# Kernel optimization log

Measured on AMD Instinct MI355X. Metric: run time of the kernel, lower is better.

The kernel has to match this reference:

```python
import jax, jax.numpy as jnp
import numpy as np

DIM = 1024
HEADS = 16
HD = DIM // HEADS          # 64
HID = 4 * DIM              # 4096
TPF = 1374                 # tokens_per_frame
LR = 0.1
NS_ITERS = 5
TTT_STEPS = 2
B, S = 2, 4
SN = S * TPF               # 5496


def _newton_schulz(G, iters=NS_ITERS):
    """Muon Newton-Schulz orthogonalization (quintic iteration)."""
    a, b, c = 3.4445, -4.7750, 2.0315
    X = G / (jnp.linalg.norm(G) + 1e-7)
    transposed = G.shape[0] > G.shape[1]
    if transposed:
        X = X.T
    for _ in range(iters):
        A = X @ X.T                      # [m,m], m = min(rows, cols)
        X = a * X + (b * A + c * (A @ A)) @ X
    return X.T if transposed else X


def _muon_update(p, g):
    return p - LR * _newton_schulz(g)


def setup_inputs() -> dict:
    key = jax.random.key(0)
    ks = jax.random.split(key, 8)
    inp = {
        "x": jax.random.normal(ks[0], (B, SN, DIM), jnp.float32),
        "qkv_w": jax.random.normal(ks[1], (DIM, 3 * DIM), jnp.float32) * (DIM ** -0.5),
        "qkv_b": jnp.zeros((3 * DIM,), jnp.float32),
        "qn_scale": jnp.ones((HD,), jnp.float32),
        "qn_bias": jnp.zeros((HD,), jnp.float32),
        "kn_scale": jnp.ones((HD,), jnp.float32),
        "kn_bias": jnp.zeros((HD,), jnp.float32),
        # theta: lecun-normal scale (std = 1/sqrt(fan_in))
        "ttt_gate": jax.random.normal(ks[2], (DIM, HID), jnp.float32) * (DIM ** -0.5),
        "ttt_val": jax.random.normal(ks[3], (DIM, HID), jnp.float32) * (DIM ** -0.5),
        "ttt_proj": jax.random.normal(ks[4], (HID, DIM), jnp.float32) * (HID ** -0.5),
        "proj_w": jax.random.normal(ks[5], (DIM, DIM), jnp.float32) * (DIM ** -0.5),
        "proj_b": jnp.zeros((DIM,), jnp.float32),
    }
    return inp


def reference(x, qkv_w, qkv_b, qn_scale, qn_bias, kn_scale, kn_bias,
              ttt_gate, ttt_val, ttt_proj, proj_w, proj_b):
    Bx, SNx, _ = x.shape
    qkv = x @ qkv_w + qkv_b                       # [B, SN, 3*DIM]
    q, k, v = jnp.split(qkv, 3, axis=-1)
    q = q.reshape(Bx, SNx, HEADS, HD)
    k = k.reshape(Bx, SNx, HEADS, HD)
    # per-head L2 normalize then affine NormLayer (x*scale + bias)
    q = q / (jnp.linalg.norm(q, axis=-1, keepdims=True) + 1e-6) * qn_scale + qn_bias
    k = k / (jnp.linalg.norm(k, axis=-1, keepdims=True) + 1e-6) * kn_scale + kn_bias
    q_ttt = q.reshape(-1, DIM)                    # [B*SN, DIM]
    k_ttt = k.reshape(-1, DIM)
    # no short_conv param at init -> v_mixed is identity, so v_target == v
    v_ttt = v.reshape(-1, DIM)

    theta = {"gate": ttt_gate, "val": ttt_val, "proj": ttt_proj}

    def loss_fn(p):
        h = jax.nn.swish(k_ttt @ p["gate"]) * (k_ttt @ p["val"])   # [B*SN, HID]
        pred = h @ p["proj"]                                        # [B*SN, DIM]
        return jnp.mean((pred - v_ttt) ** 2)

    for _ in range(TTT_STEPS):
        grads = jax.grad(loss_fn)(theta)
        theta = {kk: _muon_update(theta[kk], grads[kk]) for kk in theta}

    h_q = jax.nn.swish(q_ttt @ theta["gate"]) * (q_ttt @ theta["val"])
    o = (h_q @ theta["proj"]) @ proj_w + proj_b
    return o.reshape(Bx, SNx, DIM)
```

## Files before the change

### kernel.cpp

```cpp
#include <hip/hip_runtime.h>
#include <stdint.h>

#define NTOK 10992
#define NTOKA 11264
#define FCHK 5632
#define PMi 4194304

typedef unsigned short u16;
typedef __attribute__((ext_vector_type(8))) __bf16 b8;
typedef __attribute__((ext_vector_type(4))) float f32x4;

__device__ __forceinline__ u16 f2b(float f) {
  union { float f; uint32_t u; } v; v.f = f;
  return (u16)((v.u + 0x7fffu + ((v.u >> 16) & 1u)) >> 16);
}
__device__ __forceinline__ float b2f(u16 b) {
  union { uint32_t u; float f; } v; v.u = ((uint32_t)b) << 16; return v.f;
}
__device__ __forceinline__ uint2 pk4(u16 a, u16 b, u16 c, u16 d) {
  uint2 r; r.x = (uint32_t)a | ((uint32_t)b << 16); r.y = (uint32_t)c | ((uint32_t)d << 16);
  return r;
}
__device__ __forceinline__ void gload16(const u16* g, u16* l) {
  __builtin_amdgcn_global_load_lds((const __attribute__((address_space(1))) void*)(const void*)g,
                                   (__attribute__((address_space(3))) void*)(void*)l, 16, 0, 0);
}

struct GA {
  const u16* A[3]; const u16* B[3];
  void* C[3]; u16* O1[3]; u16* OT[3];
  const void* E0[3]; const u16* E1[3];
  int lda[3], ldb[3];
  int M, N, K, ldc, ldo1, ldt, lde0, lde1;
  float p0, p1;
};

template <int EPI, int SPLIT>
__global__ __launch_bounds__(256, 2) void gemm_bt(GA g) {
  __shared__ u16 As[128 * 32];
  __shared__ u16 Bs[128 * 32];
  int bz = blockIdx.z, koff = 0, klen = g.K;
  if constexpr (SPLIT) { koff = (bz & 1) * (g.K >> 1); bz >>= 1; klen = g.K >> 1; }
  const u16* __restrict__ A = g.A[bz] + koff;
  const u16* __restrict__ B = g.B[bz] + koff;
  const int lda = g.lda[bz], ldb = g.ldb[bz];
  const int m0 = blockIdx.y * 128, n0 = blockIdx.x * 128;
  const int tid = threadIdx.x, w = tid >> 6, lane = tid & 63;
  const int wr = (w >> 1) * 64, wc = (w & 1) * 64;
  const int ln = lane & 15, lq = lane >> 4;

  f32x4 acc[4][4];
#pragma unroll
  for (int i = 0; i < 4; ++i)
#pragma unroll
    for (int j = 0; j < 4; ++j)
#pragma unroll
      for (int r = 0; r < 4; ++r) acc[i][j][r] = 0.f;

  const u16* Ag = A + (size_t)(m0 + 32 * w + (lane >> 2)) * lda + (lane & 3) * 8;
  const u16* Bg = B + (size_t)(n0 + 32 * w + (lane >> 2)) * ldb + (lane & 3) * 8;
  u16* AsW = &As[w * 1024];
  u16* BsW = &Bs[w * 1024];
  const int nkt = klen >> 5;

  for (int kt = 0; kt < nkt; ++kt) {
    __syncthreads();
    gload16(Ag, AsW);
    gload16(Ag + (size_t)16 * lda, AsW + 512);
    gload16(Bg, BsW);
    gload16(Bg + (size_t)16 * ldb, BsW + 512);
    Ag += 32; Bg += 32;
    __syncthreads();
    b8 af[4], bfr[4];
#pragma unroll
    for (int i = 0; i < 4; ++i) af[i] = *(const b8*)&As[(wr + i * 16 + ln) * 32 + lq * 8];
#pragma unroll
    for (int j = 0; j < 4; ++j) bfr[j] = *(const b8*)&Bs[(wc + j * 16 + ln) * 32 + lq * 8];
#pragma unroll
    for (int i = 0; i < 4; ++i)
#pragma unroll
      for (int j = 0; j < 4; ++j)
        acc[i][j] = __builtin_amdgcn_mfma_f32_16x16x32_bf16(af[i], bfr[j], acc[i][j], 0, 0, 0);
  }

  float* Cf = (float*)g.C[bz];
  u16* Cb = (u16*)g.C[bz];
  u16* O1 = g.O1[bz];
  u16* OT = g.OT[bz];
  const float* E0f = (const float*)g.E0[bz];
  const u16* E0b = (const u16*)g.E0[bz];
  const u16* E1b = g.E1[bz];

#pragma unroll
  for (int i = 0; i < 4; ++i) {
    const int mb = m0 + wr + i * 16 + lq * 4;
    if (mb >= g.M) continue;
#pragma unroll
    for (int j = 0; j < 4; ++j) {
      const int n = n0 + wc + j * 16 + ln;
      if (n >= g.N) continue;
      float vv[4];
#pragma unroll
      for (int r = 0; r < 4; ++r) vv[r] = acc[i][j][r];
      if constexpr (EPI == 0) {
#pragma unroll
        for (int r = 0; r < 4; ++r) Cb[(size_t)(mb + r) * g.ldc + n] = f2b(vv[r]);
      } else if constexpr (EPI == 1) {
        const float bias = E0f[n];
#pragma unroll
        for (int r = 0; r < 4; ++r) Cb[(size_t)(mb + r) * g.ldc + n] = f2b(vv[r] + bias);
      } else if constexpr (EPI == 5) {
        u16 cq[4], oq[4];
#pragma unroll
        for (int r = 0; r < 4; ++r) {
          const int m = mb + r;
          const float zg = b2f(E0b[(size_t)m * g.lde0 + n]);
          const float zv = b2f(E1b[(size_t)m * g.lde1 + n]);
          const float s = 1.f / (1.f + __expf(-zg));
          cq[r] = f2b(vv[r] * zv * s * (1.f + zg * (1.f - s)));
          oq[r] = f2b(vv[r] * zg * s);
        }
        *(uint2*)&Cb[(size_t)n * g.ldt + mb] = pk4(cq[0], cq[1], cq[2], cq[3]);
        *(uint2*)&O1[(size_t)n * g.ldt + mb] = pk4(oq[0], oq[1], oq[2], oq[3]);
      } else if constexpr (EPI == 8) {
#pragma unroll
        for (int r = 0; r < 4; ++r) atomicAdd(&Cf[(size_t)(mb + r) * g.ldc + n], vv[r]);
      } else if constexpr (EPI == 9) {
        u16 cq[4];
#pragma unroll
        for (int r = 0; r < 4; ++r) {
          const int m = mb + r;
          const u16 ub = f2b(g.p0 * b2f(E0b[(size_t)m * g.lde0 + n]) + vv[r]);
          Cb[(size_t)m * g.ldc + n] = ub;
          cq[r] = ub;
        }
        *(uint2*)&OT[(size_t)n * g.ldt + mb] = pk4(cq[0], cq[1], cq[2], cq[3]);
      }
    }
  }
}

template <int EPI>
__global__ __launch_bounds__(256, 2) void gemm_gv(GA g) {
  __shared__ u16 As[128 * 32];
  __shared__ u16 Gs[128 * 32];
  __shared__ u16 Vs[128 * 32];
  const u16* __restrict__ A = g.A[0];
  const u16* __restrict__ G = g.B[0];
  const u16* __restrict__ V = g.B[1];
  const int lda = g.lda[0], ldb = g.ldb[0];
  const int m0 = blockIdx.y * 128, n0 = blockIdx.x * 128;
  const int tid = threadIdx.x, w = tid >> 6, lane = tid & 63;
  const int wr = (w >> 1) * 64, wc = (w & 1) * 64;
  const int ln = lane & 15, lq = lane >> 4;

  f32x4 ag[4][4], av[4][4];
#pragma unroll
  for (int i = 0; i < 4; ++i)
#pragma unroll
    for (int j = 0; j < 4; ++j)
#pragma unroll
      for (int r = 0; r < 4; ++r) { ag[i][j][r] = 0.f; av[i][j][r] = 0.f; }

  const u16* Agp = A + (size_t)(m0 + 32 * w + (lane >> 2)) * lda + (lane & 3) * 8;
  const u16* Ggp = G + (size_t)(n0 + 32 * w + (lane >> 2)) * ldb + (lane & 3) * 8;
  const u16* Vgp = V + (size_t)(n0 + 32 * w + (lane >> 2)) * ldb + (lane & 3) * 8;
  u16* AsW = &As[w * 1024];
  u16* GsW = &Gs[w * 1024];
  u16* VsW = &Vs[w * 1024];
  const int nkt = g.K >> 5;

  for (int kt = 0; kt < nkt; ++kt) {
    __syncthreads();
    gload16(Agp, AsW);
    gload16(Agp + (size_t)16 * lda, AsW + 512);
    gload16(Ggp, GsW);
    gload16(Ggp + (size_t)16 * ldb, GsW + 512);
    gload16(Vgp, VsW);
    gload16(Vgp + (size_t)16 * ldb, VsW + 512);
    Agp += 32; Ggp += 32; Vgp += 32;
    __syncthreads();
    b8 af[4], gf[4], vf[4];
#pragma unroll
    for (int i = 0; i < 4; ++i) af[i] = *(const b8*)&As[(wr + i * 16 + ln) * 32 + lq * 8];
#pragma unroll
    for (int j = 0; j < 4; ++j) gf[j] = *(const b8*)&Gs[(wc + j * 16 + ln) * 32 + lq * 8];
#pragma unroll
    for (int j = 0; j < 4; ++j) vf[j] = *(const b8*)&Vs[(wc + j * 16 + ln) * 32 + lq * 8];
#pragma unroll
    for (int i = 0; i < 4; ++i)
#pragma unroll
      for (int j = 0; j < 4; ++j) {
        ag[i][j] = __builtin_amdgcn_mfma_f32_16x16x32_bf16(af[i], gf[j], ag[i][j], 0, 0, 0);
        av[i][j] = __builtin_amdgcn_mfma_f32_16x16x32_bf16(af[i], vf[j], av[i][j], 0, 0, 0);
      }
  }

  u16* Zg = (u16*)g.C[0];
  u16* Zv = g.O1[0];
  u16* Hh = g.O1[1];
  u16* HT = g.OT[0];

#pragma unroll
  for (int i = 0; i < 4; ++i) {
    const int mb = m0 + wr + i * 16 + lq * 4;
    if (mb >= g.M) continue;
#pragma unroll
    for (int j = 0; j < 4; ++j) {
      const int n = n0 + wc + j * 16 + ln;
      if (n >= g.N) continue;
      u16 hq[4];
#pragma unroll
      for (int r = 0; r < 4; ++r) {
        const int m = mb + r;
        const float zg = ag[i][j][r];
        const float zv = av[i][j][r];
        const float s = 1.f / (1.f + __expf(-zg));
        const u16 hb = f2b(zg * s * zv);
        if constexpr (EPI == 0) {
          Zg[(size_t)m * g.ldc + n] = f2b(zg);
          Zv[(size_t)m * g.ldc + n] = f2b(zv);
          Hh[(size_t)m * g.ldc + n] = hb;
          hq[r] = hb;
        } else {
          Zg[(size_t)m * g.ldc + n] = hb;
        }
      }
      if constexpr (EPI == 0)
        *(uint2*)&HT[(size_t)n * g.ldt + mb] = pk4(hq[0], hq[1], hq[2], hq[3]);
    }
  }
}

template <int EPI>
__global__ __launch_bounds__(256, 2) void gemm64(GA g) {
  if constexpr (EPI == 10 || EPI == 11) {
    if (blockIdx.x > blockIdx.y) return;
  }
  __shared__ u16 As[64 * 32];
  __shared__ u16 Bs[64 * 32];
  const int bz = blockIdx.z;
  const u16* __restrict__ A = g.A[bz];
  const u16* __restrict__ B = g.B[bz];
  const int lda = g.lda[bz], ldb = g.ldb[bz];
  const int m0 = blockIdx.y * 64, n0 = blockIdx.x * 64;
  const int tid = threadIdx.x, w = tid >> 6, lane = tid & 63;
  const int wr = (w >> 1) * 32, wc = (w & 1) * 32;
  const int ln = lane & 15, lq = lane >> 4;

  f32x4 acc[2][2];
#pragma unroll
  for (int i = 0; i < 2; ++i)
#pragma unroll
    for (int j = 0; j < 2; ++j)
#pragma unroll
      for (int r = 0; r < 4; ++r) acc[i][j][r] = 0.f;

  const u16* Ag = A + (size_t)(m0 + 16 * w + (lane >> 2)) * lda + (lane & 3) * 8;
  const u16* Bg = B + (size_t)(n0 + 16 * w + (lane >> 2)) * ldb + (lane & 3) * 8;
  u16* AsW = &As[w * 512];
  u16* BsW = &Bs[w * 512];
  const int nkt = g.K >> 5;

  for (int kt = 0; kt < nkt; ++kt) {
    __syncthreads();
    gload16(Ag, AsW);
    gload16(Bg, BsW);
    Ag += 32; Bg += 32;
    __syncthreads();
    b8 af[2], bfr[2];
#pragma unroll
    for (int i = 0; i < 2; ++i) af[i] = *(const b8*)&As[(wr + i * 16 + ln) * 32 + lq * 8];
#pragma unroll
    for (int j = 0; j < 2; ++j) bfr[j] = *(const b8*)&Bs[(wc + j * 16 + ln) * 32 + lq * 8];
#pragma unroll
    for (int i = 0; i < 2; ++i)
#pragma unroll
      for (int j = 0; j < 2; ++j)
        acc[i][j] = __builtin_amdgcn_mfma_f32_16x16x32_bf16(af[i], bfr[j], acc[i][j], 0, 0, 0);
  }

  float* Cf = (float*)g.C[bz];
  u16* Cb = (u16*)g.C[bz];
  u16* OT = g.OT[bz];
  const float* E0f = (const float*)g.E0[bz];
  const u16* E0b = (const u16*)g.E0[bz];
  const bool offdiag = (blockIdx.x != blockIdx.y);

#pragma unroll
  for (int i = 0; i < 2; ++i) {
    const int mb = m0 + wr + i * 16 + lq * 4;
    if (mb >= g.M) continue;
#pragma unroll
    for (int j = 0; j < 2; ++j) {
      const int n = n0 + wc + j * 16 + ln;
      if (n >= g.N) continue;
      float vv[4];
#pragma unroll
      for (int r = 0; r < 4; ++r) vv[r] = acc[i][j][r];
      if constexpr (EPI == 0) {
#pragma unroll
        for (int r = 0; r < 4; ++r) Cb[(size_t)(mb + r) * g.ldc + n] = f2b(vv[r]);
      } else if constexpr (EPI == 2) {
        u16 cq[4];
#pragma unroll
        for (int r = 0; r < 4; ++r) {
          const int m = mb + r;
          const u16 ub = f2b((vv[r] - b2f(E0b[(size_t)m * g.lde0 + n])) * g.p0);
          Cb[(size_t)m * g.ldc + n] = ub;
          cq[r] = ub;
        }
        *(uint2*)&OT[(size_t)n * g.ldt + mb] = pk4(cq[0], cq[1], cq[2], cq[3]);
      } else if constexpr (EPI == 6) {
        const float bias = E0f[n];
#pragma unroll
        for (int r = 0; r < 4; ++r) Cf[(size_t)(mb + r) * g.ldc + n] = vv[r] + bias;
      } else if constexpr (EPI == 10) {
        u16 cq[4];
#pragma unroll
        for (int r = 0; r < 4; ++r) {
          cq[r] = f2b(vv[r]);
          Cb[(size_t)(mb + r) * g.ldc + n] = cq[r];
        }
        if (offdiag)
          *(uint2*)&Cb[(size_t)n * g.ldc + mb] = pk4(cq[0], cq[1], cq[2], cq[3]);
      } else if constexpr (EPI == 11) {
        u16 cq[4];
#pragma unroll
        for (int r = 0; r < 4; ++r) {
          cq[r] = f2b(g.p0 * b2f(E0b[(size_t)(mb + r) * g.lde0 + n]) + g.p1 * vv[r]);
          Cb[(size_t)(mb + r) * g.ldc + n] = cq[r];
        }
        if (offdiag)
          *(uint2*)&Cb[(size_t)n * g.ldc + mb] = pk4(cq[0], cq[1], cq[2], cq[3]);
      }
    }
  }
}

__global__ __launch_bounds__(256) void norm_qkv(const u16* __restrict__ qkvB,
    const float* __restrict__ qs, const float* __restrict__ qbi,
    const float* __restrict__ ks, const float* __restrict__ kbi,
    u16* __restrict__ qb, u16* __restrict__ kb, u16* __restrict__ vb) {
  const int tok = blockIdx.x;
  const int t = threadIdx.x;
  const int d = t * 4;
  const u16* row = qkvB + (size_t)tok * 3072;
  const uint2 qu = *(const uint2*)(row + d);
  const uint2 ku = *(const uint2*)(row + 1024 + d);
  *(uint2*)(vb + (size_t)tok * 1024 + d) = *(const uint2*)(row + 2048 + d);
  float q0 = b2f(qu.x & 0xffff), q1 = b2f(qu.x >> 16), q2 = b2f(qu.y & 0xffff), q3 = b2f(qu.y >> 16);
  float k0 = b2f(ku.x & 0xffff), k1 = b2f(ku.x >> 16), k2 = b2f(ku.y & 0xffff), k3 = b2f(ku.y >> 16);
  float sq = q0 * q0 + q1 * q1 + q2 * q2 + q3 * q3;
  float sk = k0 * k0 + k1 * k1 + k2 * k2 + k3 * k3;
  for (int off = 1; off < 16; off <<= 1) { sq += __shfl_xor(sq, off); sk += __shfl_xor(sk, off); }
  const float rq = 1.f / (sqrtf(sq) + 1e-6f);
  const float rk = 1.f / (sqrtf(sk) + 1e-6f);
  const int hd = d & 63;
  const float4 qsv = *(const float4*)(qs + hd);
  const float4 qbv = *(const float4*)(qbi + hd);
  const float4 ksv = *(const float4*)(ks + hd);
  const float4 kbv = *(const float4*)(kbi + hd);
  uint64_t pq = (uint64_t)f2b(q0 * rq * qsv.x + qbv.x)
              | ((uint64_t)f2b(q1 * rq * qsv.y + qbv.y) << 16)
              | ((uint64_t)f2b(q2 * rq * qsv.z + qbv.z) << 32)
              | ((uint64_t)f2b(q3 * rq * qsv.w + qbv.w) << 48);
  uint64_t pk = (uint64_t)f2b(k0 * rk * ksv.x + kbv.x)
              | ((uint64_t)f2b(k1 * rk * ksv.y + kbv.y) << 16)
              | ((uint64_t)f2b(k2 * rk * ksv.z + kbv.z) << 32)
              | ((uint64_t)f2b(k3 * rk * ksv.w + kbv.w) << 48);
  *(uint64_t*)(qb + (size_t)tok * 1024 + d) = pq;
  *(uint64_t*)(kb + (size_t)tok * 1024 + d) = pk;
}

__global__ __launch_bounds__(256) void tr_b16(const u16* __restrict__ in, u16* __restrict__ out,
                                              int Cin, int Rtot, int Rval,
                                              size_t inStr, size_t outStr) {
  const int b = blockIdx.z;
  in += (size_t)b * inStr; out += (size_t)b * outStr;
  __shared__ u16 t[32][33];
  const int c0 = blockIdx.x * 32, r0 = blockIdx.y * 32;
  const int tx = threadIdx.x, ty = threadIdx.y;
#pragma unroll
  for (int yy = 0; yy < 4; ++yy) {
    const int rr = ty * 4 + yy;
    const int r = r0 + rr;
    t[rr][tx] = (r < Rval) ? in[(size_t)r * Cin + c0 + tx] : (u16)0;
  }
  __syncthreads();
#pragma unroll
  for (int yy = 0; yy < 4; ++yy) {
    const int cc = ty * 4 + yy;
    out[(size_t)(c0 + cc) * Rtot + r0 + tx] = t[tx][cc];
  }
}

__global__ __launch_bounds__(256) void tr_f32b(const float* __restrict__ in, u16* __restrict__ out,
                                               int Cin, int Rtot) {
  __shared__ u16 t[32][33];
  const int c0 = blockIdx.x * 32, r0 = blockIdx.y * 32;
  const int tx = threadIdx.x, ty = threadIdx.y;
#pragma unroll
  for (int yy = 0; yy < 4; ++yy) {
    const int rr = ty * 4 + yy;
    t[rr][tx] = f2b(in[(size_t)(r0 + rr) * Cin + c0 + tx]);
  }
  __syncthreads();
#pragma unroll
  for (int yy = 0; yy < 4; ++yy) {
    const int cc = ty * 4 + yy;
    out[(size_t)(c0 + cc) * Rtot + r0 + tx] = t[tx][cc];
  }
}

__global__ void cvt_k(const float* __restrict__ in, u16* __restrict__ out, int n) {
  const int i = blockIdx.x * 256 + threadIdx.x;
  if (i < n) out[i] = f2b(in[i]);
}

__global__ void diag_k(float* __restrict__ out, int n, float val) {
  const int i = blockIdx.x * 256 + threadIdx.x;
  if (i < n) out[i] = val;
}

__global__ __launch_bounds__(256) void sumsq_k(const float* __restrict__ g, float* __restrict__ out) {
  const int b = blockIdx.y;
  const float* p = g + (size_t)b * PMi;
  float s = 0.f;
  for (int i = blockIdx.x * 256 + threadIdx.x; i < PMi; i += gridDim.x * 256) {
    float v = p[i]; s += v * v;
  }
  for (int off = 32; off > 0; off >>= 1) s += __shfl_xor(s, off);
  __shared__ float red[4];
  if ((threadIdx.x & 63) == 0) red[threadIdx.x >> 6] = s;
  __syncthreads();
  if (threadIdx.x == 0) atomicAdd(out + b, red[0] + red[1] + red[2] + red[3]);
}

__global__ __launch_bounds__(256) void scale_k(const float* __restrict__ g, const float* __restrict__ ss,
                                               u16* __restrict__ Xb) {
  const int b = blockIdx.y;
  const float r = 1.f / (sqrtf(ss[b]) + 1e-7f);
  const size_t o = (size_t)b * PMi;
  for (int i = blockIdx.x * 256 + threadIdx.x; i < PMi; i += gridDim.x * 256)
    Xb[o + i] = f2b(g[o + i] * r);
}

__global__ __launch_bounds__(256) void muon_apply(const u16* __restrict__ Xb_,
    u16* __restrict__ Gt, u16* __restrict__ Vt, u16* __restrict__ Pt, u16* __restrict__ Pb) {
  const int b = blockIdx.z;
  __shared__ float xs[32][33];
  __shared__ u16 ns[32][33];
  const int j0 = blockIdx.x * 32;
  const int i0 = blockIdx.y * 32;
  const u16* X = Xb_ + (size_t)b * PMi;
  const int tx = threadIdx.x, ty = threadIdx.y;
#pragma unroll
  for (int yy = 0; yy < 4; ++yy) {
    const int r = ty * 4 + yy;
    xs[r][tx] = b2f(X[(size_t)(i0 + r) * 4096 + j0 + tx]);
  }
  __syncthreads();
  if (b < 2) {
    u16* T = b ? Vt : Gt;
#pragma unroll
    for (int yy = 0; yy < 4; ++yy) {
      const int rr = ty * 4 + yy;
      const size_t idx = (size_t)(j0 + rr) * 1024 + i0 + tx;
      T[idx] = f2b(b2f(T[idx]) - 0.1f * xs[tx][rr]);
    }
  } else {
#pragma unroll
    for (int yy = 0; yy < 4; ++yy) {
      const int rr = ty * 4 + yy;
      const size_t idx = (size_t)(j0 + rr) * 1024 + i0 + tx;
      const float nv = b2f(Pb[idx]) - 0.1f * xs[tx][rr];
      const u16 nb = f2b(nv);
      Pb[idx] = nb;
      ns[rr][tx] = nb;
    }
    __syncthreads();
#pragma unroll
    for (int yy = 0; yy < 4; ++yy) {
      const int rr = ty * 4 + yy;
      Pt[(size_t)(i0 + rr) * 4096 + j0 + tx] = ns[tx][rr];
    }
  }
}

static GA mk(const u16* A, const u16* B, void* C, int M, int N, int K,
             int lda, int ldb, int ldc) {
  GA a{};
  a.A[0] = a.A[1] = a.A[2] = A;
  a.B[0] = a.B[1] = a.B[2] = B;
  a.C[0] = a.C[1] = a.C[2] = C;
  a.lda[0] = a.lda[1] = a.lda[2] = lda;
  a.ldb[0] = a.ldb[1] = a.ldb[2] = ldb;
  a.M = M; a.N = N; a.K = K; a.ldc = ldc;
  return a;
}

extern "C" void kernel_launch(void* const* d_in, const int* in_sizes, int n_in,
                              void* d_out, int out_size, void* d_ws, size_t ws_size,
                              hipStream_t stream) {
  (void)in_sizes; (void)n_in;
  const float* x      = (const float*)d_in[0];
  const float* qkv_w  = (const float*)d_in[1];
  const float* qkv_b  = (const float*)d_in[2];
  const float* qn_s   = (const float*)d_in[3];
  const float* qn_b   = (const float*)d_in[4];
  const float* kn_s   = (const float*)d_in[5];
  const float* kn_b   = (const float*)d_in[6];
  const float* g_gate = (const float*)d_in[7];
  const float* g_val  = (const float*)d_in[8];
  const float* g_proj = (const float*)d_in[9];
  const float* proj_w = (const float*)d_in[10];
  const float* proj_b = (const float*)d_in[11];
  float* out = (float*)d_out;

  const size_t PM = PMi;
  const size_t TD = (size_t)NTOKA * 1024;

  const size_t NEED1 = 253231360 + 4096;
  const size_t NEED2 = 127926528 + 177209344 + 4096;
  if (ws_size < NEED1) {
    diag_k<<<dim3((out_size + 255) / 256), dim3(256), 0, stream>>>(out, out_size,
                                                                   (float)(ws_size >> 20));
    return;
  }
  const int CHKr = (ws_size >= NEED2) ? 2816 : 1408;

  char* p = (char*)d_ws;
  auto carve = [&](size_t bytes) { char* r = p; p += (bytes + 255) & ~(size_t)255; return (void*)r; };
  auto cdiv = [](int a, int b) { return (a + b - 1) / b; };

  u16* Gt     = (u16*)carve(PM * 2);
  u16* Vt     = (u16*)carve(PM * 2);
  u16* Pt     = (u16*)carve(PM * 2);
  u16* Pb     = (u16*)carve(PM * 2);
  u16* projWt = (u16*)carve(1048576ull * 2);
  u16* qb     = (u16*)carve(TD * 2);
  u16* kb     = (u16*)carve(TD * 2);
  u16* vT     = (u16*)carve(TD * 2);
  u16* kT     = (u16*)carve(TD * 2);
  float* ssq  = (float*)carve(256);
  char* arena = p;

  u16* xb     = (u16*)arena;
  u16* qkvWt  = (u16*)(arena + 23068672);
  u16* qkvB   = (u16*)(arena + 29360128);
  u16* vb_tmp = (u16*)(arena + 96894976);
  const size_t CB = (size_t)CHKr * 4096 * 2;
  const size_t DP = (size_t)CHKr * 1024 * 2;
  u16* zg     = (u16*)arena;
  u16* zv     = (u16*)(arena + CB);
  u16* hh     = (u16*)(arena + 2 * CB);
  u16* hT     = (u16*)(arena + 3 * CB);
  u16* dzvT   = (u16*)(arena + 4 * CB);
  u16* dpredT = (u16*)(arena + 5 * CB);
  u16* dpredb = (u16*)(arena + 5 * CB + DP);
  float* gAll = (float*)(arena + 5 * CB + 2 * DP);
  u16* XAb  = (u16*)arena;
  u16* XAbT = (u16*)(arena + 25165824);
  u16* XBb  = (u16*)(arena + 50331648);
  u16* XBbT = (u16*)(arena + 75497472);
  u16* Ab   = (u16*)(arena + 100663296);
  u16* Wb   = (u16*)(arena + 106954752);
  const int FCN  = (CHKr >= 2816) ? 1 : 2;
  const int FBLK = (FCN == 1) ? NTOK : FCHK;
  u16* hbuf = (u16*)arena;
  u16* oc   = (u16*)(arena + ((FCN == 1) ? 92274688ull : 46137344ull));

  const dim3 blk(256), tb32(32, 8);
  const float inv2 = 2.0f / (10992.0f * 1024.0f);
  const float nsa = 3.4445f, nsb = -4.7750f, nsc = 2.0315f;

  cvt_k<<<dim3(43968), blk, 0, stream>>>(x, xb, NTOK * 1024);
  cvt_k<<<dim3(16384), blk, 0, stream>>>(g_proj, Pb, (int)PM);
  tr_f32b<<<dim3(96, 32), tb32, 0, stream>>>(qkv_w, qkvWt, 3072, 1024);
  tr_f32b<<<dim3(32, 32), tb32, 0, stream>>>(proj_w, projWt, 1024, 1024);
  tr_f32b<<<dim3(128, 32), tb32, 0, stream>>>(g_gate, Gt, 4096, 1024);
  tr_f32b<<<dim3(128, 32), tb32, 0, stream>>>(g_val, Vt, 4096, 1024);
  tr_f32b<<<dim3(32, 128), tb32, 0, stream>>>(g_proj, Pt, 1024, 4096);

  {
    GA a = mk(xb, qkvWt, qkvB, NTOK, 3072, 1024, 1024, 1024, 3072);
    a.E0[0] = a.E0[1] = a.E0[2] = qkv_b;
    gemm_bt<1, 0><<<dim3(24, 86, 1), blk, 0, stream>>>(a);
  }
  norm_qkv<<<dim3(NTOK), blk, 0, stream>>>(qkvB, qn_s, qn_b, kn_s, kn_b, qb, kb, vb_tmp);
  tr_b16<<<dim3(32, 352, 1), tb32, 0, stream>>>(kb, kT, 1024, NTOKA, NTOK, 0, 0);
  tr_b16<<<dim3(32, 352, 1), tb32, 0, stream>>>(vb_tmp, vT, 1024, NTOKA, NTOK, 0, 0);

  for (int step = 0; step < 2; ++step) {
    hipMemsetAsync(gAll, 0, 3 * PM * 4, stream);
    for (int c0 = 0; c0 < NTOK; c0 += CHKr) {
      const int vc = (NTOK - c0 < CHKr) ? (NTOK - c0) : CHKr;
      const int mt = cdiv(vc, 128);
      const u16* kc = kb + (size_t)c0 * 1024;
      if (vc < CHKr)
        hipMemsetAsync(hT, 0, 2 * CB + DP, stream);
      {
        GA a{};
        a.A[0] = kc; a.lda[0] = 1024;
        a.B[0] = Gt; a.B[1] = Vt; a.ldb[0] = 1024;
        a.C[0] = zg; a.O1[0] = zv; a.O1[1] = hh; a.OT[0] = hT;
        a.M = vc; a.N = 4096; a.K = 1024; a.ldc = 4096; a.ldt = CHKr;
        gemm_gv<0><<<dim3(32, mt, 1), blk, 0, stream>>>(a);
      }
      {
        GA a = mk(Pt, hh, dpredT, 1024, vc, 4096, 4096, 4096, CHKr);
        a.OT[0] = dpredb; a.ldt = 1024;
        a.E0[0] = vT + c0; a.lde0 = NTOKA; a.p0 = inv2;
        gemm64<2><<<dim3(cdiv(vc, 64), 16, 1), blk, 0, stream>>>(a);
      }
      if (vc < CHKr)
        hipMemsetAsync(hh, 0, CB, stream);
      {
        GA a = mk(dpredb, Pb, hh, vc, 4096, 1024, 1024, 1024, 0);
        a.O1[0] = dzvT; a.ldt = CHKr;
        a.E0[0] = zg; a.lde0 = 4096; a.E1[0] = zv; a.lde1 = 4096;
        gemm_bt<5, 0><<<dim3(32, mt, 1), blk, 0, stream>>>(a);
      }
      {
        GA a{};
        a.A[0] = kT + c0; a.A[1] = kT + c0; a.A[2] = dpredT;
        a.lda[0] = NTOKA; a.lda[1] = NTOKA; a.lda[2] = CHKr;
        a.B[0] = hh; a.B[1] = dzvT; a.B[2] = hT;
        a.ldb[0] = a.ldb[1] = a.ldb[2] = CHKr;
        a.C[0] = gAll; a.C[1] = gAll + PM; a.C[2] = gAll + 2 * PM;
        a.M = 1024; a.N = 4096; a.K = CHKr; a.ldc = 4096;
        gemm_bt<8, 1><<<dim3(32, 8, 6), blk, 0, stream>>>(a);
      }
    }
    hipMemsetAsync(ssq, 0, 16, stream);
    sumsq_k<<<dim3(512, 3), blk, 0, stream>>>(gAll, ssq);
    scale_k<<<dim3(2048, 3), blk, 0, stream>>>(gAll, ssq, XAb);
    tr_b16<<<dim3(128, 32, 3), tb32, 0, stream>>>(XAb, XAbT, 4096, 1024, 1024, PM, PM);

    u16* Xi_b = XAb; u16* Xi_bT = XAbT;
    u16* Xo_b = XBb; u16* Xo_bT = XBbT;
    for (int it = 0; it < 5; ++it) {
      {
        GA a{};
        for (int b = 0; b < 3; ++b) {
          a.A[b] = Xi_b + (size_t)b * PM; a.B[b] = Xi_b + (size_t)b * PM;
          a.C[b] = Ab + (size_t)b * 1048576;
          a.lda[b] = 4096; a.ldb[b] = 4096;
        }
        a.M = 1024; a.N = 1024; a.K = 4096; a.ldc = 1024;
        gemm64<10><<<dim3(16, 16, 3), blk, 0, stream>>>(a);
      }
      {
        GA a{};
        for (int b = 0; b < 3; ++b) {
          a.A[b] = Ab + (size_t)b * 1048576; a.B[b] = Ab + (size_t)b * 1048576;
          a.C[b] = Wb + (size_t)b * 1048576; a.E0[b] = Ab + (size_t)b * 1048576;
          a.lda[b] = 1024; a.ldb[b] = 1024;
        }
        a.M = 1024; a.N = 1024; a.K = 1024; a.ldc = 1024; a.lde0 = 1024;
        a.p0 = nsb; a.p1 = nsc;
        gemm64<11><<<dim3(16, 16, 3), blk, 0, stream>>>(a);
      }
      {
        GA a{};
        for (int b = 0; b < 3; ++b) {
          a.A[b] = Wb + (size_t)b * 1048576; a.B[b] = Xi_bT + (size_t)b * PM;
          a.C[b] = Xo_b + (size_t)b * PM; a.OT[b] = Xo_bT + (size_t)b * PM;
          a.E0[b] = Xi_b + (size_t)b * PM;
          a.lda[b] = 1024; a.ldb[b] = 1024;
        }
        a.M = 1024; a.N = 4096; a.K = 1024; a.ldc = 4096; a.ldt = 1024;
        a.lde0 = 4096; a.p0 = nsa;
        gemm_bt<9, 0><<<dim3(32, 8, 3), blk, 0, stream>>>(a);
      }
      u16* tb = Xi_b; Xi_b = Xo_b; Xo_b = tb;
      u16* tt = Xi_bT; Xi_bT = Xo_bT; Xo_bT = tt;
    }
    muon_apply<<<dim3(128, 32, 3), tb32, 0, stream>>>(Xi_b, Gt, Vt, Pt, Pb);
  }

  for (int fc = 0; fc < FCN; ++fc) {
    const int c0 = fc * FBLK;
    const int vc = (NTOK - c0 < FBLK) ? (NTOK - c0) : FBLK;
    const int mt = cdiv(vc, 128), mt64 = cdiv(vc, 64);
    const u16* qc = qb + (size_t)c0 * 1024;
    {
      GA a{};
      a.A[0] = qc; a.lda[0] = 1024;
      a.B[0] = Gt; a.B[1] = Vt; a.ldb[0] = 1024;
      a.C[0] = hbuf;
      a.M = vc; a.N = 4096; a.K = 1024; a.ldc = 4096;
      gemm_gv<1><<<dim3(32, mt, 1), blk, 0, stream>>>(a);
    }
    gemm64<0><<<dim3(16, mt64, 1), blk, 0, stream>>>(
        mk(hbuf, Pt, oc, vc, 1024, 4096, 4096, 4096, 1024));
    {
      GA a = mk(oc, projWt, out + (size_t)c0 * 1024, vc, 1024, 1024, 1024, 1024, 1024);
      a.E0[0] = proj_b;
      gemm64<6><<<dim3(16, mt64, 1), blk, 0, stream>>>(a);
    }
  }
}
```

Before: 6.333 ms.

## Update Newton-Schulz Gram matrix algebraically and pair gradient GEMM with next chunk

Newton-Schulz no longer recomputes X·Xᵀ with K=4096 on each iteration. It updates A algebraically as a²A + a(WA + (WA)ᵀ) + WAW using two 1024-sized GEMMs, which is less work but lets bf16 rounding error accumulate in A across iterations. When workspace allows, the weight-gradient GEMM of one token chunk is held back and launched in the same grid as the next chunk's gate/value GEMM, with double-buffered h buffers, to reduce launch count and fill the GPU better. The transposed output write is also skipped on the final iteration.

```diff
diff --git a/kernel.cpp b/kernel.cpp
--- a/kernel.cpp
+++ b/kernel.cpp
@@ -134,7 +134,7 @@
           Cb[(size_t)m * g.ldc + n] = ub;
           cq[r] = ub;
         }
-        *(uint2*)&OT[(size_t)n * g.ldt + mb] = pk4(cq[0], cq[1], cq[2], cq[3]);
+        if (OT) *(uint2*)&OT[(size_t)n * g.ldt + mb] = pk4(cq[0], cq[1], cq[2], cq[3]);
       }
     }
   }
@@ -232,9 +232,146 @@
   }
 }
 
+__global__ __launch_bounds__(256, 2) void fused_gg(GA ggr, GA ggv, int ysplit) {
+  __shared__ u16 As[128 * 32];
+  __shared__ u16 Bs[128 * 32];
+  __shared__ u16 Vs[128 * 32];
+  const int tid = threadIdx.x, w = tid >> 6, lane = tid & 63;
+  const int wr = (w >> 1) * 64, wc = (w & 1) * 64;
+  const int ln = lane & 15, lq = lane >> 4;
+
+  if ((int)blockIdx.y < ysplit) {
+    const u16* __restrict__ A = ggv.A[0];
+    const u16* __restrict__ G = ggv.B[0];
+    const u16* __restrict__ V = ggv.B[1];
+    const int lda = ggv.lda[0], ldb = ggv.ldb[0];
+    const int m0 = blockIdx.y * 128, n0 = blockIdx.x * 128;
+    f32x4 ag[4][4], av[4][4];
+#pragma unroll
+    for (int i = 0; i < 4; ++i)
+#pragma unroll
+      for (int j = 0; j < 4; ++j)
+#pragma unroll
+        for (int r = 0; r < 4; ++r) { ag[i][j][r] = 0.f; av[i][j][r] = 0.f; }
+    const u16* Agp = A + (size_t)(m0 + 32 * w + (lane >> 2)) * lda + (lane & 3) * 8;
+    const u16* Ggp = G + (size_t)(n0 + 32 * w + (lane >> 2)) * ldb + (lane & 3) * 8;
+    const u16* Vgp = V + (size_t)(n0 + 32 * w + (lane >> 2)) * ldb + (lane & 3) * 8;
+    u16* AsW = &As[w * 1024];
+    u16* GsW = &Bs[w * 1024];
+    u16* VsW = &Vs[w * 1024];
+    const int nkt = ggv.K >> 5;
+    for (int kt = 0; kt < nkt; ++kt) {
+      __syncthreads();
+      gload16(Agp, AsW);
+      gload16(Agp + (size_t)16 * lda, AsW + 512);
+      gload16(Ggp, GsW);
+      gload16(Ggp + (size_t)16 * ldb, GsW + 512);
+      gload16(Vgp, VsW);
+      gload16(Vgp + (size_t)16 * ldb, VsW + 512);
+      Agp += 32; Ggp += 32; Vgp += 32;
+      __syncthreads();
+      b8 af[4], gf[4], vf[4];
+#pragma unroll
+      for (int i = 0; i < 4; ++i) af[i] = *(const b8*)&As[(wr + i * 16 + ln) * 32 + lq * 8];
+#pragma unroll
+      for (int j = 0; j < 4; ++j) gf[j] = *(const b8*)&Bs[(wc + j * 16 + ln) * 32 + lq * 8];
+#pragma unroll
+      for (int j = 0; j < 4; ++j) vf[j] = *(const b8*)&Vs[(wc + j * 16 + ln) * 32 + lq * 8];
+#pragma unroll
+      for (int i = 0; i < 4; ++i)
+#pragma unroll
+        for (int j = 0; j < 4; ++j) {
+          ag[i][j] = __builtin_amdgcn_mfma_f32_16x16x32_bf16(af[i], gf[j], ag[i][j], 0, 0, 0);
+          av[i][j] = __builtin_amdgcn_mfma_f32_16x16x32_bf16(af[i], vf[j], av[i][j], 0, 0, 0);
+        }
+    }
+    u16* Zg = (u16*)ggv.C[0];
+    u16* Zv = ggv.O1[0];
+    u16* Hh = ggv.O1[1];
+    u16* HT = ggv.OT[0];
+#pragma unroll
+    for (int i = 0; i < 4; ++i) {
+      const int mb = m0 + wr + i * 16 + lq * 4;
+      if (mb >= ggv.M) continue;
+#pragma unroll
+      for (int j = 0; j < 4; ++j) {
+        const int n = n0 + wc + j * 16 + ln;
+        if (n >= ggv.N) continue;
+        u16 hq[4];
+#pragma unroll
+        for (int r = 0; r < 4; ++r) {
+          const int m = mb + r;
+          const float zg = ag[i][j][r];
+          const float zv = av[i][j][r];
+          const float s = 1.f / (1.f + __expf(-zg));
+          const u16 hb = f2b(zg * s * zv);
+          Zg[(size_t)m * ggv.ldc + n] = f2b(zg);
+          Zv[(size_t)m * ggv.ldc + n] = f2b(zv);
+          Hh[(size_t)m * ggv.ldc + n] = hb;
+          hq[r] = hb;
+        }
+        *(uint2*)&HT[(size_t)n * ggv.ldt + mb] = pk4(hq[0], hq[1], hq[2], hq[3]);
+      }
+    }
+  } else {
+    const int yy = (int)blockIdx.y - ysplit;
+    int bz = yy >> 3;
+    const int m0 = (yy & 7) * 128, n0 = blockIdx.x * 128;
+    const int koff = (bz & 1) * (ggr.K >> 1); bz >>= 1;
+    const int klen = ggr.K >> 1;
+    const u16* __restrict__ A = ggr.A[bz] + koff;
+    const u16* __restrict__ B = ggr.B[bz] + koff;
+    const int lda = ggr.lda[bz], ldb = ggr.ldb[bz];
+    f32x4 acc[4][4];
+#pragma unroll
+    for (int i = 0; i < 4; ++i)
+#pragma unroll
+      for (int j = 0; j < 4; ++j)
+#pragma unroll
+        for (int r = 0; r < 4; ++r) acc[i][j][r] = 0.f;
+    const u16* Ag = A + (size_t)(m0 + 32 * w + (lane >> 2)) * lda + (lane & 3) * 8;
+    const u16* Bg = B + (size_t)(n0 + 32 * w + (lane >> 2)) * ldb + (lane & 3) * 8;
+    u16* AsW = &As[w * 1024];
+    u16* BsW = &Bs[w * 1024];
+    const int nkt = klen >> 5;
+    for (int kt = 0; kt < nkt; ++kt) {
+      __syncthreads();
+      gload16(Ag, AsW);
+      gload16(Ag + (size_t)16 * lda, AsW + 512);
+      gload16(Bg, BsW);
+      gload16(Bg + (size_t)16 * ldb, BsW + 512);
+      Ag += 32; Bg += 32;
+      __syncthreads();
+      b8 af[4], bfr[4];
+#pragma unroll
+      for (int i = 0; i < 4; ++i) af[i] = *(const b8*)&As[(wr + i * 16 + ln) * 32 + lq * 8];
+#pragma unroll
+      for (int j = 0; j < 4; ++j) bfr[j] = *(const b8*)&Bs[(wc + j * 16 + ln) * 32 + lq * 8];
+#pragma unroll
+      for (int i = 0; i < 4; ++i)
+#pragma unroll
+        for (int j = 0; j < 4; ++j)
+          acc[i][j] = __builtin_amdgcn_mfma_f32_16x16x32_bf16(af[i], bfr[j], acc[i][j], 0, 0, 0);
+    }
+    float* Cf = (float*)ggr.C[bz];
+#pragma unroll
+    for (int i = 0; i < 4; ++i) {
+      const int mb = m0 + wr + i * 16 + lq * 4;
+      if (mb >= ggr.M) continue;
+#pragma unroll
+      for (int j = 0; j < 4; ++j) {
+        const int n = n0 + wc + j * 16 + ln;
+        if (n >= ggr.N) continue;
+#pragma unroll
+        for (int r = 0; r < 4; ++r) atomicAdd(&Cf[(size_t)(mb + r) * ggr.ldc + n], acc[i][j][r]);
+      }
+    }
+  }
+}
+
 template <int EPI>
 __global__ __launch_bounds__(256, 2) void gemm64(GA g) {
-  if constexpr (EPI == 10 || EPI == 11) {
+  if constexpr (EPI == 10 || EPI == 11 || EPI == 12) {
     if (blockIdx.x > blockIdx.y) return;
   }
   __shared__ u16 As[64 * 32];
@@ -285,6 +422,7 @@
   u16* OT = g.OT[bz];
   const float* E0f = (const float*)g.E0[bz];
   const u16* E0b = (const u16*)g.E0[bz];
+  const u16* E1b = g.E1[bz];
   const bool offdiag = (blockIdx.x != blockIdx.y);
 
 #pragma unroll
@@ -330,6 +468,21 @@
         for (int r = 0; r < 4; ++r) {
           cq[r] = f2b(g.p0 * b2f(E0b[(size_t)(mb + r) * g.lde0 + n]) + g.p1 * vv[r]);
           Cb[(size_t)(mb + r) * g.ldc + n] = cq[r];
+        }
+        if (offdiag)
+          *(uint2*)&Cb[(size_t)n * g.ldc + mb] = pk4(cq[0], cq[1], cq[2], cq[3]);
+      } else if constexpr (EPI == 12) {
+        const uint2 t2u = *(const uint2*)&E1b[(size_t)n * g.lde1 + mb];
+        const float t2v[4] = { b2f((u16)(t2u.x & 0xffff)), b2f((u16)(t2u.x >> 16)),
+                               b2f((u16)(t2u.y & 0xffff)), b2f((u16)(t2u.y >> 16)) };
+        u16 cq[4];
+#pragma unroll
+        for (int r = 0; r < 4; ++r) {
+          const int m = mb + r;
+          const float t1 = b2f(E1b[(size_t)m * g.lde1 + n]);
+          const float a0 = b2f(E0b[(size_t)m * g.lde0 + n]);
+          cq[r] = f2b(g.p0 * a0 + g.p1 * (t1 + t2v[r]) + vv[r]);
+          Cb[(size_t)m * g.ldc + n] = cq[r];
         }
         if (offdiag)
           *(uint2*)&Cb[(size_t)n * g.ldc + mb] = pk4(cq[0], cq[1], cq[2], cq[3]);
@@ -523,12 +676,14 @@
 
   const size_t NEED1 = 253231360 + 4096;
   const size_t NEED2 = 127926528 + 177209344 + 4096;
+  const size_t NEEDP = 351273216 + 8192;
   if (ws_size < NEED1) {
     diag_k<<<dim3((out_size + 255) / 256), dim3(256), 0, stream>>>(out, out_size,
                                                                    (float)(ws_size >> 20));
     return;
   }
   const int CHKr = (ws_size >= NEED2) ? 2816 : 1408;
+  const int PAIRED = (ws_size >= NEEDP) ? 1 : 0;
 
   char* p = (char*)d_ws;
   auto carve = [&](size_t bytes) { char* r = p; p += (bytes + 255) & ~(size_t)255; return (void*)r; };
@@ -554,18 +709,23 @@
   const size_t DP = (size_t)CHKr * 1024 * 2;
   u16* zg     = (u16*)arena;
   u16* zv     = (u16*)(arena + CB);
-  u16* hh     = (u16*)(arena + 2 * CB);
-  u16* hT     = (u16*)(arena + 3 * CB);
+  u16* hh0    = (u16*)(arena + 2 * CB);
+  u16* hT0    = (u16*)(arena + 3 * CB);
   u16* dzvT   = (u16*)(arena + 4 * CB);
   u16* dpredT = (u16*)(arena + 5 * CB);
   u16* dpredb = (u16*)(arena + 5 * CB + DP);
   float* gAll = (float*)(arena + 5 * CB + 2 * DP);
+  u16* hh1    = PAIRED ? (u16*)(arena + 5 * CB + 2 * DP + 3 * PM * 4) : hh0;
+  u16* hT1    = PAIRED ? (u16*)(arena + 6 * CB + 2 * DP + 3 * PM * 4) : hT0;
+  u16* hhA[2] = {hh0, hh1};
+  u16* hTA[2] = {hT0, hT1};
   u16* XAb  = (u16*)arena;
   u16* XAbT = (u16*)(arena + 25165824);
   u16* XBb  = (u16*)(arena + 50331648);
   u16* XBbT = (u16*)(arena + 75497472);
   u16* Ab   = (u16*)(arena + 100663296);
   u16* Wb   = (u16*)(arena + 106954752);
+  u16* Tb   = (u16*)(arena + 113246208);
   const int FCN  = (CHKr >= 2816) ? 1 : 2;
   const int FBLK = (FCN == 1) ? NTOK : FCHK;
   u16* hbuf = (u16*)arena;
@@ -594,30 +754,43 @@
 
   for (int step = 0; step < 2; ++step) {
     hipMemsetAsync(gAll, 0, 3 * PM * 4, stream);
-    for (int c0 = 0; c0 < NTOK; c0 += CHKr) {
+    int havePend = 0;
+    GA pendGA{};
+    for (int ci = 0, c0 = 0; c0 < NTOK; ++ci, c0 += CHKr) {
       const int vc = (NTOK - c0 < CHKr) ? (NTOK - c0) : CHKr;
       const int mt = cdiv(vc, 128);
       const u16* kc = kb + (size_t)c0 * 1024;
+      u16* hhp = hhA[ci & 1];
+      u16* hTp = hTA[ci & 1];
       if (vc < CHKr)
-        hipMemsetAsync(hT, 0, 2 * CB + DP, stream);
+        hipMemsetAsync(hTp, 0, CB, stream);
       {
-        GA a{};
-        a.A[0] = kc; a.lda[0] = 1024;
-        a.B[0] = Gt; a.B[1] = Vt; a.ldb[0] = 1024;
-        a.C[0] = zg; a.O1[0] = zv; a.O1[1] = hh; a.OT[0] = hT;
-        a.M = vc; a.N = 4096; a.K = 1024; a.ldc = 4096; a.ldt = CHKr;
-        gemm_gv<0><<<dim3(32, mt, 1), blk, 0, stream>>>(a);
+        GA agv{};
+        agv.A[0] = kc; agv.lda[0] = 1024;
+        agv.B[0] = Gt; agv.B[1] = Vt; agv.ldb[0] = 1024;
+        agv.C[0] = zg; agv.O1[0] = zv; agv.O1[1] = hhp; agv.OT[0] = hTp;
+        agv.M = vc; agv.N = 4096; agv.K = 1024; agv.ldc = 4096; agv.ldt = CHKr;
+        if (PAIRED && havePend) {
+          fused_gg<<<dim3(32, mt + 48, 1), blk, 0, stream>>>(pendGA, agv, mt);
+          havePend = 0;
+        } else {
+          gemm_gv<0><<<dim3(32, mt, 1), blk, 0, stream>>>(agv);
+        }
+      }
+      if (vc < CHKr) {
+        hipMemsetAsync(dzvT, 0, CB, stream);
+        hipMemsetAsync(dpredT, 0, DP, stream);
       }
       {
-        GA a = mk(Pt, hh, dpredT, 1024, vc, 4096, 4096, 4096, CHKr);
+        GA a = mk(Pt, hhp, dpredT, 1024, vc, 4096, 4096, 4096, CHKr);
         a.OT[0] = dpredb; a.ldt = 1024;
         a.E0[0] = vT + c0; a.lde0 = NTOKA; a.p0 = inv2;
         gemm64<2><<<dim3(cdiv(vc, 64), 16, 1), blk, 0, stream>>>(a);
       }
       if (vc < CHKr)
-        hipMemsetAsync(hh, 0, CB, stream);
+        hipMemsetAsync(hhp, 0, CB, stream);
       {
-        GA a = mk(dpredb, Pb, hh, vc, 4096, 1024, 1024, 1024, 0);
+        GA a = mk(dpredb, Pb, hhp, vc, 4096, 1024, 1024, 1024, 0);
         a.O1[0] = dzvT; a.ldt = CHKr;
         a.E0[0] = zg; a.lde0 = 4096; a.E1[0] = zv; a.lde1 = 4096;
         gemm_bt<5, 0><<<dim3(32, mt, 1), blk, 0, stream>>>(a);
@@ -626,11 +799,13 @@
         GA a{};
         a.A[0] = kT + c0; a.A[1] = kT + c0; a.A[2] = dpredT;
         a.lda[0] = NTOKA; a.lda[1] = NTOKA; a.lda[2] = CHKr;
-        a.B[0] = hh; a.B[1] = dzvT; a.B[2] = hT;
+        a.B[0] = hhp; a.B[1] = dzvT; a.B[2] = hTp;
         a.ldb[0] = a.ldb[1] = a.ldb[2] = CHKr;
         a.C[0] = gAll; a.C[1] = gAll + PM; a.C[2] = gAll + 2 * PM;
         a.M = 1024; a.N = 4096; a.K = CHKr; a.ldc = 4096;
-        gemm_bt<8, 1><<<dim3(32, 8, 6), blk, 0, stream>>>(a);
+        const int last = (c0 + CHKr >= NTOK);
+        if (PAIRED && !last) { pendGA = a; havePend = 1; }
+        else gemm_bt<8, 1><<<dim3(32, 8, 6), blk, 0, stream>>>(a);
       }
     }
     hipMemsetAsync(ssq, 0, 16, stream);
@@ -640,17 +815,17 @@
 
     u16* Xi_b = XAb; u16* Xi_bT = XAbT;
     u16* Xo_b = XBb; u16* Xo_bT = XBbT;
+    {
+      GA a{};
+      for (int b = 0; b < 3; ++b) {
+        a.A[b] = Xi_b + (size_t)b * PM; a.B[b] = Xi_b + (size_t)b * PM;
+        a.C[b] = Ab + (size_t)b * 1048576;
+        a.lda[b] = 4096; a.ldb[b] = 4096;
+      }
+      a.M = 1024; a.N = 1024; a.K = 4096; a.ldc = 1024;
+      gemm64<10><<<dim3(16, 16, 3), blk, 0, stream>>>(a);
+    }
     for (int it = 0; it < 5; ++it) {
-      {
-        GA a{};
-        for (int b = 0; b < 3; ++b) {
-          a.A[b] = Xi_b + (size_t)b * PM; a.B[b] = Xi_b + (size_t)b * PM;
-          a.C[b] = Ab + (size_t)b * 1048576;
-          a.lda[b] = 4096; a.ldb[b] = 4096;
-        }
-        a.M = 1024; a.N = 1024; a.K = 4096; a.ldc = 1024;
-        gemm64<10><<<dim3(16, 16, 3), blk, 0, stream>>>(a);
-      }
       {
         GA a{};
         for (int b = 0; b < 3; ++b) {
@@ -666,13 +841,39 @@
         GA a{};
         for (int b = 0; b < 3; ++b) {
           a.A[b] = Wb + (size_t)b * 1048576; a.B[b] = Xi_bT + (size_t)b * PM;
-          a.C[b] = Xo_b + (size_t)b * PM; a.OT[b] = Xo_bT + (size_t)b * PM;
+          a.C[b] = Xo_b + (size_t)b * PM;
+          a.OT[b] = (it == 4) ? nullptr : (Xo_bT + (size_t)b * PM);
           a.E0[b] = Xi_b + (size_t)b * PM;
           a.lda[b] = 1024; a.ldb[b] = 1024;
         }
         a.M = 1024; a.N = 4096; a.K = 1024; a.ldc = 4096; a.ldt = 1024;
         a.lde0 = 4096; a.p0 = nsa;
         gemm_bt<9, 0><<<dim3(32, 8, 3), blk, 0, stream>>>(a);
+      }
+      if (it < 4) {
+        {
+          GA a{};
+          for (int b = 0; b < 3; ++b) {
+            a.A[b] = Wb + (size_t)b * 1048576; a.B[b] = Ab + (size_t)b * 1048576;
+            a.C[b] = Tb + (size_t)b * 1048576;
+            a.lda[b] = 1024; a.ldb[b] = 1024;
+          }
+          a.M = 1024; a.N = 1024; a.K = 1024; a.ldc = 1024;
+          gemm64<0><<<dim3(16, 16, 3), blk, 0, stream>>>(a);
+        }
+        {
+          GA a{};
+          for (int b = 0; b < 3; ++b) {
+            a.A[b] = Tb + (size_t)b * 1048576; a.B[b] = Wb + (size_t)b * 1048576;
+            a.C[b] = Ab + (size_t)b * 1048576;
+            a.E0[b] = Ab + (size_t)b * 1048576; a.E1[b] = Tb + (size_t)b * 1048576;
+            a.lda[b] = 1024; a.ldb[b] = 1024;
+          }
+          a.M = 1024; a.N = 1024; a.K = 1024; a.ldc = 1024;
+          a.lde0 = 1024; a.lde1 = 1024;
+          a.p0 = nsa * nsa; a.p1 = nsa;
+          gemm64<12><<<dim3(16, 16, 3), blk, 0, stream>>>(a);
+        }
       }
       u16* tb = Xi_b; Xi_b = Xo_b; Xo_b = tb;
       u16* tt = Xi_bT; Xi_bT = Xo_bT; Xo_bT = tt;
```

Result: faster. 6.079 ms (-4.0%).
